# Kernel tuning notes

Measured on AMD Instinct MI355X. Metric: run time of the kernel, lower is better.

Reference implementation:

```python
import jax, jax.numpy as jnp
import numpy as np

N = 50000
E = 800000
IN_FEATS = 128
OUT_FEATS = 64
ALPHA = 0.2  # LeakyReLU negative slope


def setup_inputs() -> dict:
    key = jax.random.key(0)
    k1, k2, k3, k4, k5 = jax.random.split(key, 5)
    h = jax.random.normal(k1, (N, IN_FEATS), dtype=jnp.float32)
    src = jax.random.randint(k2, (E,), 0, N)
    dst = jax.random.randint(k3, (E,), 0, N)
    edge_index = jnp.stack([src, dst], axis=0).astype(jnp.int64)
    # xavier_uniform with gain=1.414
    limW = 1.414 * np.sqrt(6.0 / (IN_FEATS + OUT_FEATS))
    W = jax.random.uniform(k4, (IN_FEATS, OUT_FEATS), dtype=jnp.float32, minval=-limW, maxval=limW)
    lima = 1.414 * np.sqrt(6.0 / (2 * OUT_FEATS + 1))
    a = jax.random.uniform(k5, (2 * OUT_FEATS, 1), dtype=jnp.float32, minval=-lima, maxval=lima)
    return {"h": h, "edge_index": edge_index, "W": W, "a": a}


def reference(h, edge_index, W, a):
    src, dst = edge_index[0], edge_index[1]
    Wh = h @ W                               # (N, out)
    # split attention vector: cat([Wh_src, Wh_dst]) @ a == Wh_src@a1 + Wh_dst@a2
    a1 = a[:OUT_FEATS, 0]                    # (out,)
    a2 = a[OUT_FEATS:, 0]                    # (out,)
    s1 = Wh @ a1                             # (N,)
    s2 = Wh @ a2                             # (N,)
    e = jax.nn.leaky_relu(s1[src] + s2[dst], negative_slope=ALPHA)  # (E,)
    exp_e = jnp.exp(e)
    denom = jax.ops.segment_sum(exp_e, dst, num_segments=N)          # (N,)
    attention = exp_e / denom[dst]                                   # (E,)
    # dropout p=0.0 / eval mode -> identity
    msgs = attention[:, None] * Wh[src]                              # (E, out)
    h_prime = jax.ops.segment_sum(msgs, dst, num_segments=N)         # (N, out)
    return jax.nn.elu(h_prime)
```

## Files before the change

kernel.cpp:

```cpp
#include <hip/hip_runtime.h>
#include <math.h>

#define GN 50000
#define GE 800000
#define INF 128
#define OUTF 64
#define LRELU_ALPHA 0.2f

#define BUCK_SH 5
#define BUCKW   32
#define NB      ((GN + BUCKW - 1) / BUCKW)
#define GT      ((GN + 63) / 64)
#define CHUNK   4096
#define NCH     ((GE + CHUNK - 1) / CHUNK)
#define CAP     768

__device__ __forceinline__ unsigned short f32_to_bf16(float f) {
    unsigned int u = __float_as_uint(f);
    return (unsigned short)((u + 0x7fffu + ((u >> 16) & 1u)) >> 16);
}
__device__ __forceinline__ float bf16lo(unsigned int u) { return __uint_as_float(u << 16); }
__device__ __forceinline__ float bf16hi(unsigned int u) { return __uint_as_float(u & 0xffff0000u); }

__global__ __launch_bounds__(256) void k_front(const float* __restrict__ h,
                                               const float* __restrict__ W,
                                               const float* __restrict__ a,
                                               const int* __restrict__ src,
                                               const int* __restrict__ dst,
                                               unsigned short* __restrict__ Whb,
                                               float* __restrict__ s1,
                                               float* __restrict__ s2,
                                               int* __restrict__ ccount,
                                               int* __restrict__ epacked) {
    __shared__ __align__(16) float Wlds[INF * OUTF];
    int t = threadIdx.x;

    if (blockIdx.x < NCH) {
        int* hist = (int*)Wlds;
        int* run  = hist + NB;
        for (int i = t; i < NB; i += 256) hist[i] = 0;
        __syncthreads();

        int base = blockIdx.x * CHUNK;
        int pk[CHUNK / 256];
        int bb[CHUNK / 256];
        #pragma unroll
        for (int i = 0; i < CHUNK / 256; ++i) {
            int e = base + i * 256 + t;
            if (e < GE) {
                int d = dst[e];
                int b = d >> BUCK_SH;
                pk[i] = (src[e] << BUCK_SH) | (d & (BUCKW - 1));
                bb[i] = b;
                atomicAdd(&hist[b], 1);
            } else {
                bb[i] = -1;
            }
        }
        __syncthreads();
        for (int i = t; i < NB; i += 256) {
            int c = hist[i];
            if (c > 0) run[i] = i * CAP + atomicAdd(&ccount[i], c);
        }
        __syncthreads();
        #pragma unroll
        for (int i = 0; i < CHUNK / 256; ++i) {
            if (bb[i] >= 0) {
                int pos = atomicAdd(&run[bb[i]], 1);
                epacked[pos] = pk[i];
            }
        }
    } else {
        for (int i = t * 4; i < INF * OUTF; i += 256 * 4)
            *(float4*)&Wlds[i] = *(const float4*)&W[i];
        __syncthreads();

        int fg = t & 15;
        int ng = t >> 4;
        int jg = fg * 4;
        int n0 = (blockIdx.x - NCH) * 64 + ng * 4;

        int m0 = n0 + 0 < GN ? n0 + 0 : GN - 1;
        int m1 = n0 + 1 < GN ? n0 + 1 : GN - 1;
        int m2 = n0 + 2 < GN ? n0 + 2 : GN - 1;
        int m3 = n0 + 3 < GN ? n0 + 3 : GN - 1;
        const float* h0 = &h[m0 * INF];
        const float* h1 = &h[m1 * INF];
        const float* h2 = &h[m2 * INF];
        const float* h3 = &h[m3 * INF];

        float4 acc0 = {0.f,0.f,0.f,0.f}, acc1 = acc0, acc2 = acc0, acc3 = acc0;
        for (int kc = 0; kc < INF; kc += 4) {
            float4 hv0 = *(const float4*)&h0[kc];
            float4 hv1 = *(const float4*)&h1[kc];
            float4 hv2 = *(const float4*)&h2[kc];
            float4 hv3 = *(const float4*)&h3[kc];
            #pragma unroll
            for (int kk = 0; kk < 4; ++kk) {
                float4 wv = *(float4*)&Wlds[(kc + kk) * OUTF + jg];
                float a0 = ((const float*)&hv0)[kk];
                float a1v = ((const float*)&hv1)[kk];
                float a2v = ((const float*)&hv2)[kk];
                float a3 = ((const float*)&hv3)[kk];
                acc0.x += a0 * wv.x; acc0.y += a0 * wv.y; acc0.z += a0 * wv.z; acc0.w += a0 * wv.w;
                acc1.x += a1v * wv.x; acc1.y += a1v * wv.y; acc1.z += a1v * wv.z; acc1.w += a1v * wv.w;
                acc2.x += a2v * wv.x; acc2.y += a2v * wv.y; acc2.z += a2v * wv.z; acc2.w += a2v * wv.w;
                acc3.x += a3 * wv.x; acc3.y += a3 * wv.y; acc3.z += a3 * wv.z; acc3.w += a3 * wv.w;
            }
        }

        float4 accs[4] = {acc0, acc1, acc2, acc3};
        #pragma unroll
        for (int i = 0; i < 4; ++i) {
            if (n0 + i < GN) {
                ushort4 p;
                p.x = f32_to_bf16(accs[i].x); p.y = f32_to_bf16(accs[i].y);
                p.z = f32_to_bf16(accs[i].z); p.w = f32_to_bf16(accs[i].w);
                *(ushort4*)&Whb[(n0 + i) * OUTF + jg] = p;
            }
        }

        float4 va1 = *(const float4*)&a[jg];
        float4 va2 = *(const float4*)&a[OUTF + jg];
        float p1[4], p2[4];
        #pragma unroll
        for (int i = 0; i < 4; ++i) {
            p1[i] = accs[i].x * va1.x + accs[i].y * va1.y + accs[i].z * va1.z + accs[i].w * va1.w;
            p2[i] = accs[i].x * va2.x + accs[i].y * va2.y + accs[i].z * va2.z + accs[i].w * va2.w;
        }
        #pragma unroll
        for (int off = 8; off >= 1; off >>= 1) {
            #pragma unroll
            for (int i = 0; i < 4; ++i) {
                p1[i] += __shfl_down(p1[i], off, 16);
                p2[i] += __shfl_down(p2[i], off, 16);
            }
        }
        if (fg == 0) {
            #pragma unroll
            for (int i = 0; i < 4; ++i) {
                if (n0 + i < GN) { s1[n0 + i] = p1[i]; s2[n0 + i] = p2[i]; }
            }
        }
    }
}

__global__ __launch_bounds__(256) void k_fgather(const int* __restrict__ ccount,
                                                 const int* __restrict__ epacked,
                                                 const float* __restrict__ s1,
                                                 const float* __restrict__ s2,
                                                 const unsigned short* __restrict__ Whb,
                                                 float* __restrict__ out) {
    __shared__ int2 sorted2[CAP];
    __shared__ int hist[BUCKW];
    __shared__ int cur[BUCKW];
    __shared__ int cstart[BUCKW + 1];
    __shared__ float s2l[BUCKW];

    int t = threadIdx.x;
    int b = blockIdx.x;
    int dstbase = b * BUCKW;
    int nd = GN - dstbase; if (nd > BUCKW) nd = BUCKW;

    if (t < BUCKW) {
        hist[t] = 0;
        s2l[t] = (t < nd) ? s2[dstbase + t] : 0.f;
    }
    __syncthreads();

    int cnt = ccount[b]; if (cnt > CAP) cnt = CAP;
    const int* row = &epacked[b * CAP];

    int pkr[CAP / 256]; float exr[CAP / 256];
    #pragma unroll
    for (int it = 0; it < CAP / 256; ++it) {
        int i = t + it * 256;
        if (i < cnt) {
            int pk = row[i];
            pkr[it] = pk;
            atomicAdd(&hist[pk & (BUCKW - 1)], 1);
            float x = s1[pk >> BUCK_SH] + s2l[pk & (BUCKW - 1)];
            x = (x > 0.f) ? x : LRELU_ALPHA * x;
            exr[it] = __expf(x);
        }
    }
    __syncthreads();

    if (t < BUCKW) {
        int v = hist[t];
        int incl = v;
        #pragma unroll
        for (int off = 1; off < BUCKW; off <<= 1) {
            int u = __shfl_up(incl, off, BUCKW);
            if (t >= off) incl += u;
        }
        cstart[t + 1] = incl;
        cur[t] = incl - v;
        if (t == 0) cstart[0] = 0;
    }
    __syncthreads();

    #pragma unroll
    for (int it = 0; it < CAP / 256; ++it) {
        int i = t + it * 256;
        if (i < cnt) {
            int pos = atomicAdd(&cur[pkr[it] & (BUCKW - 1)], 1);
            sorted2[pos] = make_int2(pkr[it], __float_as_int(exr[it]));
        }
    }
    __syncthreads();

    int grp  = t >> 3;
    int lane = t & 7;
    int jg   = lane * 8;
    int dl   = grp;
    int c0 = cstart[dl], c1 = cstart[dl + 1];
    float acc[8] = {0.f,0.f,0.f,0.f,0.f,0.f,0.f,0.f};
    float den = 0.f;
    for (int cb = c0; cb < c1; cb += 8) {
        int m = c1 - cb; if (m > 8) m = 8;
        int   sj[8]; float exj[8];
        #pragma unroll
        for (int j = 0; j < 8; ++j) {
            if (j < m) {
                int2 pe = sorted2[cb + j];
                sj[j]  = pe.x >> BUCK_SH;
                exj[j] = __uint_as_float(pe.y);
            }
        }
        uint4 wv[8];
        #pragma unroll
        for (int j = 0; j < 8; ++j)
            if (j < m) wv[j] = *(const uint4*)&Whb[sj[j] * OUTF + jg];
        #pragma unroll
        for (int j = 0; j < 8; ++j) {
            if (j < m) {
                float ex = exj[j];
                den += ex;
                acc[0] += ex * bf16lo(wv[j].x); acc[1] += ex * bf16hi(wv[j].x);
                acc[2] += ex * bf16lo(wv[j].y); acc[3] += ex * bf16hi(wv[j].y);
                acc[4] += ex * bf16lo(wv[j].z); acc[5] += ex * bf16hi(wv[j].z);
                acc[6] += ex * bf16lo(wv[j].w); acc[7] += ex * bf16hi(wv[j].w);
            }
        }
    }
    if (dl < nd) {
        float inv = (c1 > c0) ? 1.f / den : 0.f;
        float o[8];
        #pragma unroll
        for (int j = 0; j < 8; ++j) {
            float v = acc[j] * inv;
            o[j] = (v > 0.f) ? v : expm1f(v);
        }
        float* op = &out[(dstbase + dl) * OUTF + jg];
        *(float4*)(op + 0) = make_float4(o[0], o[1], o[2], o[3]);
        *(float4*)(op + 4) = make_float4(o[4], o[5], o[6], o[7]);
    }
}

extern "C" void kernel_launch(void* const* d_in, const int* in_sizes, int n_in,
                              void* d_out, int out_size, void* d_ws, size_t ws_size,
                              hipStream_t stream) {
    const float* h  = (const float*)d_in[0];
    const int*   ei = (const int*)d_in[1];
    const float* W  = (const float*)d_in[2];
    const float* a  = (const float*)d_in[3];
    const int* src = ei;
    const int* dst = ei + GE;

    float* ws = (float*)d_ws;
    float* s1 = ws;
    float* s2 = s1 + GN;
    unsigned short* Whb = (unsigned short*)(s2 + GN);
    int* epacked = (int*)(Whb + (size_t)GN * OUTF);
    int* ccount  = epacked + (size_t)NB * CAP;
    float* out = (float*)d_out;

    hipMemsetAsync(ccount, 0, NB * sizeof(int), stream);
    k_front<<<NCH + GT, 256, 0, stream>>>(h, W, a, src, dst, Whb, s1, s2,
                                          ccount, epacked);
    k_fgather<<<NB, 256, 0, stream>>>(ccount, epacked, s1, s2, Whb, out);
}
```

Before: 120.8 us.

## Replace per-bucket counting sort with LDS float atomic accumulation per edge

The gather kernel no longer sorts each bucket's edges by destination with a histogram, scan and scatter. Each thread now handles one edge at a time, loads the full 64-wide bf16 source row and atomically adds the weighted values and the softmax denominator into a shared-memory accumulator for its destination. This removes two barriers and the sort stages, but adds 65 LDS float atomics per edge plus contention, and each thread reads an entire 128-byte row instead of cooperative 16-byte slices. Float atomics also make the summation order nondeterministic.

```diff
diff --git a/kernel.cpp b/kernel.cpp
--- a/kernel.cpp
+++ b/kernel.cpp
@@ -151,10 +151,8 @@
                                                  const float* __restrict__ s2,
                                                  const unsigned short* __restrict__ Whb,
                                                  float* __restrict__ out) {
-    __shared__ int2 sorted2[CAP];
-    __shared__ int hist[BUCKW];
-    __shared__ int cur[BUCKW];
-    __shared__ int cstart[BUCKW + 1];
+    __shared__ float accS[BUCKW][OUTF + 1];
+    __shared__ float denS[BUCKW];
     __shared__ float s2l[BUCKW];
 
     int t = threadIdx.x;
@@ -162,8 +160,10 @@
     int dstbase = b * BUCKW;
     int nd = GN - dstbase; if (nd > BUCKW) nd = BUCKW;
 
+    for (int i = t; i < BUCKW * (OUTF + 1); i += 256)
+        ((float*)accS)[i] = 0.f;
     if (t < BUCKW) {
-        hist[t] = 0;
+        denS[t] = 0.f;
         s2l[t] = (t < nd) ? s2[dstbase + t] : 0.f;
     }
     __syncthreads();
@@ -171,88 +171,47 @@
     int cnt = ccount[b]; if (cnt > CAP) cnt = CAP;
     const int* row = &epacked[b * CAP];
 
-    int pkr[CAP / 256]; float exr[CAP / 256];
-    #pragma unroll
-    for (int it = 0; it < CAP / 256; ++it) {
-        int i = t + it * 256;
-        if (i < cnt) {
-            int pk = row[i];
-            pkr[it] = pk;
-            atomicAdd(&hist[pk & (BUCKW - 1)], 1);
-            float x = s1[pk >> BUCK_SH] + s2l[pk & (BUCKW - 1)];
-            x = (x > 0.f) ? x : LRELU_ALPHA * x;
-            exr[it] = __expf(x);
+    for (int i = t; i < cnt; i += 256) {
+        int pk = row[i];
+        int d  = pk & (BUCKW - 1);
+        int sI = pk >> BUCK_SH;
+        float x = s1[sI] + s2l[d];
+        x = (x > 0.f) ? x : LRELU_ALPHA * x;
+        float ex = __expf(x);
+
+        const uint4* wp = (const uint4*)&Whb[sI * OUTF];
+        uint4 wv[8];
+        #pragma unroll
+        for (int q = 0; q < 8; ++q) wv[q] = wp[q];
+
+        atomicAdd(&denS[d], ex);
+        float* ar = accS[d];
+        #pragma unroll
+        for (int q = 0; q < 8; ++q) {
+            atomicAdd(&ar[q * 8 + 0], ex * bf16lo(wv[q].x));
+            atomicAdd(&ar[q * 8 + 1], ex * bf16hi(wv[q].x));
+            atomicAdd(&ar[q * 8 + 2], ex * bf16lo(wv[q].y));
+            atomicAdd(&ar[q * 8 + 3], ex * bf16hi(wv[q].y));
+            atomicAdd(&ar[q * 8 + 4], ex * bf16lo(wv[q].z));
+            atomicAdd(&ar[q * 8 + 5], ex * bf16hi(wv[q].z));
+            atomicAdd(&ar[q * 8 + 6], ex * bf16lo(wv[q].w));
+            atomicAdd(&ar[q * 8 + 7], ex * bf16hi(wv[q].w));
         }
     }
     __syncthreads();
 
-    if (t < BUCKW) {
-        int v = hist[t];
-        int incl = v;
-        #pragma unroll
-        for (int off = 1; off < BUCKW; off <<= 1) {
-            int u = __shfl_up(incl, off, BUCKW);
-            if (t >= off) incl += u;
-        }
-        cstart[t + 1] = incl;
-        cur[t] = incl - v;
-        if (t == 0) cstart[0] = 0;
-    }
-    __syncthreads();
-
-    #pragma unroll
-    for (int it = 0; it < CAP / 256; ++it) {
-        int i = t + it * 256;
-        if (i < cnt) {
-            int pos = atomicAdd(&cur[pkr[it] & (BUCKW - 1)], 1);
-            sorted2[pos] = make_int2(pkr[it], __float_as_int(exr[it]));
-        }
-    }
-    __syncthreads();
-
-    int grp  = t >> 3;
-    int lane = t & 7;
-    int jg   = lane * 8;
-    int dl   = grp;
-    int c0 = cstart[dl], c1 = cstart[dl + 1];
-    float acc[8] = {0.f,0.f,0.f,0.f,0.f,0.f,0.f,0.f};
-    float den = 0.f;
-    for (int cb = c0; cb < c1; cb += 8) {
-        int m = c1 - cb; if (m > 8) m = 8;
-        int   sj[8]; float exj[8];
+    int d  = t >> 3;
+    int jg = (t & 7) * 8;
+    if (d < nd) {
+        float den = denS[d];
+        float inv = (den > 0.f) ? 1.f / den : 0.f;
+        float o[8];
         #pragma unroll
         for (int j = 0; j < 8; ++j) {
-            if (j < m) {
-                int2 pe = sorted2[cb + j];
-                sj[j]  = pe.x >> BUCK_SH;
-                exj[j] = __uint_as_float(pe.y);
-            }
-        }
-        uint4 wv[8];
-        #pragma unroll
-        for (int j = 0; j < 8; ++j)
-            if (j < m) wv[j] = *(const uint4*)&Whb[sj[j] * OUTF + jg];
-        #pragma unroll
-        for (int j = 0; j < 8; ++j) {
-            if (j < m) {
-                float ex = exj[j];
-                den += ex;
-                acc[0] += ex * bf16lo(wv[j].x); acc[1] += ex * bf16hi(wv[j].x);
-                acc[2] += ex * bf16lo(wv[j].y); acc[3] += ex * bf16hi(wv[j].y);
-                acc[4] += ex * bf16lo(wv[j].z); acc[5] += ex * bf16hi(wv[j].z);
-                acc[6] += ex * bf16lo(wv[j].w); acc[7] += ex * bf16hi(wv[j].w);
-            }
-        }
-    }
-    if (dl < nd) {
-        float inv = (c1 > c0) ? 1.f / den : 0.f;
-        float o[8];
-        #pragma unroll
-        for (int j = 0; j < 8; ++j) {
-            float v = acc[j] * inv;
+            float v = accS[d][jg + j] * inv;
             o[j] = (v > 0.f) ? v : expm1f(v);
         }
-        float* op = &out[(dstbase + dl) * OUTF + jg];
+        float* op = &out[(dstbase + d) * OUTF + jg];
         *(float4*)(op + 0) = make_float4(o[0], o[1], o[2], o[3]);
         *(float4*)(op + 4) = make_float4(o[4], o[5], o[6], o[7]);
     }
```

Result: slower. 410.3 us (+239.6%).
